# Performance work log

Hardware: AMD Instinct MI355X
Metric: run time of the kernel (lower is better)

The kernel has to match this reference:

```python
import jax, jax.numpy as jnp
import numpy as np

D_MODEL = 512
NUM_HEADS = 8
WINDOW = 64
HEAD_DIM = D_MODEL // NUM_HEADS


def setup_inputs() -> dict:
    key = jax.random.key(0)
    k1, k2, k3 = jax.random.split(key, 3)
    B, F, L, D = 4, 16, 2048, D_MODEL
    x = jax.random.normal(k1, (B, F, L, D), dtype=jnp.float32)
    w_qkv = jax.random.normal(k2, (D, 3 * D), dtype=jnp.float32) * (1.0 / np.sqrt(D))
    b_qkv = jnp.zeros((3 * D,), dtype=jnp.float32)
    w_proj = jax.random.normal(k3, (D, D), dtype=jnp.float32) * (1.0 / np.sqrt(D))
    b_proj = jnp.zeros((D,), dtype=jnp.float32)
    return {"x": x, "w_qkv": w_qkv, "b_qkv": b_qkv, "w_proj": w_proj, "b_proj": b_proj}


def reference(x, w_qkv, b_qkv, w_proj, b_proj):
    B, F, L, D = x.shape
    W = WINDOW
    H, hd = NUM_HEADS, HEAD_DIM
    nw = L // W  # L chosen divisible by window_size; pad path is identity here
    # partition into windows: (B, F, nw, W, D)
    xw = x.reshape(B, F, nw, W, D)
    # fused QKV projection
    qkv = jnp.einsum('bfnwd,de->bfnwe', xw, w_qkv) + b_qkv  # (B,F,nw,W,3D)
    qkv = qkv.reshape(B, F, nw, W, 3, H, hd)
    q = qkv[..., 0, :, :]  # (B,F,nw,W,H,hd)
    k = qkv[..., 1, :, :]
    v = qkv[..., 2, :, :]
    scale = 1.0 / np.sqrt(hd).astype(np.float32)
    # per-window attention: scores (B,F,nw,H,W,W)
    scores = jnp.einsum('bfnqhd,bfnkhd->bfnhqk', q, k) * scale
    attn = jax.nn.softmax(scores, axis=-1)
    out = jnp.einsum('bfnhqk,bfnkhd->bfnqhd', attn, v)  # (B,F,nw,W,H,hd)
    out = out.reshape(B, F, nw, W, D)
    out = jnp.einsum('bfnwd,de->bfnwe', out, w_proj) + b_proj
    return out.reshape(B, F, L, D)
```

## Files before the change

kernel.cpp:

```cpp
#include <hip/hip_runtime.h>

typedef __attribute__((ext_vector_type(8))) short short8;
typedef __attribute__((ext_vector_type(4))) float f32x4;
typedef unsigned short u16;
typedef unsigned int u32;

__device__ __forceinline__ u16 f2bf(float f){
  union { float f; u32 u; } v; v.f = f;
  u32 u = v.u;
  u32 r = (u + 0x7FFFu + ((u >> 16) & 1u)) >> 16;
  return (u16)r;
}

__device__ __forceinline__ u32 cvtpk(float a, float b){
  u32 r;
  asm("v_cvt_pk_bf16_f32 %0, %1, %2" : "=v"(r) : "v"(a), "v"(b));
  return r;
}

__device__ __forceinline__ int swz(int row, int cb){ return cb ^ ((row & 7) << 4); }

__device__ __forceinline__ void gload16(const void* g, void* l){
  __builtin_amdgcn_global_load_lds(
      (const __attribute__((address_space(1))) unsigned int*)g,
      (__attribute__((address_space(3))) unsigned int*)l, 16, 0, 0);
}

__global__ void convert_weights_swz(const float* __restrict__ wqkv,
                                    const float* __restrict__ wproj,
                                    u16* __restrict__ wq_swz,
                                    u16* __restrict__ wpt){
  int c = blockIdx.x * 256 + threadIdx.x;
  union { u16 u[8]; uint4 v; } t;
  if (c < 98304){
    int tile = c >> 10, row = (c >> 3) & 127, c7 = c & 7;
    int bn = tile >> 3, kt = tile & 7;
    int j  = c7 ^ (row & 7);
    int e  = bn * 128 + row;
    int k0 = kt * 64 + j * 8;
    #pragma unroll
    for (int i = 0; i < 8; ++i) t.u[i] = f2bf(wqkv[(long)(k0 + i) * 1536 + e]);
    *reinterpret_cast<uint4*>(wq_swz + (long)c * 8) = t.v;
  } else {
    int t2 = c - 98304;
    int cc = t2 >> 6;
    int kc = (t2 & 63) << 3;
    #pragma unroll
    for (int i = 0; i < 8; ++i) t.u[i] = f2bf(wproj[(long)(kc + i) * 512 + cc]);
    *reinterpret_cast<uint4*>(wpt + (long)cc * 512 + kc) = t.v;
  }
}

__global__ void convert_x(const float* __restrict__ x, u16* __restrict__ xbf){
  int c = blockIdx.x * 256 + threadIdx.x;
  int tile = c >> 10, row = (c >> 3) & 127, c7 = c & 7;
  int bm = tile >> 3, kt = tile & 7;
  int j  = c7 ^ (row & 7);
  const float* src = x + (long)(bm * 128 + row) * 512 + kt * 64 + j * 8;
  float4 v0 = *reinterpret_cast<const float4*>(src);
  float4 v1 = *reinterpret_cast<const float4*>(src + 4);
  union { u16 u[8]; uint4 v; } t;
  t.u[0] = f2bf(v0.x); t.u[1] = f2bf(v0.y); t.u[2] = f2bf(v0.z); t.u[3] = f2bf(v0.w);
  t.u[4] = f2bf(v1.x); t.u[5] = f2bf(v1.y); t.u[6] = f2bf(v1.z); t.u[7] = f2bf(v1.w);
  *reinterpret_cast<uint4*>(xbf + (long)c * 8) = t.v;
}

__global__ __launch_bounds__(256) void qkv_gemm(
    const u16*  __restrict__ xbf,
    const u16*  __restrict__ wswz,
    const float* __restrict__ bqkv,
    u16* __restrict__ qkv)
{
  __shared__ char smem[34816];
  char* ldsA = smem;
  char* ldsB = smem + 16384;
  u16*  ldsC = (u16*)smem;

  int hb   = blockIdx.x;
  int work = (hb & 7) * 1536 + (hb >> 3);
  int bn   = work % 12;
  int bm   = work / 12;

  const int tid = threadIdx.x;
  const int l = tid & 63, w = tid >> 6;
  const int g = l >> 4,  ln = l & 15;
  const int wm = w >> 1, wn = w & 1;

  f32x4 acc[4][4];
  #pragma unroll
  for (int m = 0; m < 4; ++m)
    #pragma unroll
    for (int n = 0; n < 4; ++n) acc[m][n] = (f32x4){0.f,0.f,0.f,0.f};

  const char* abase = (const char*)(xbf  + (long)(bm * 8) * 8192);
  const char* bbase = (const char*)(wswz + (long)(bn * 8) * 8192);

  for (int kt = 0; kt < 8; ++kt){
    __syncthreads();
    #pragma unroll
    for (int i = 0; i < 4; ++i){
      gload16(abase + (long)kt*16384 + (i*256 + tid)*16, ldsA + (i*256 + w*64)*16);
      gload16(bbase + (long)kt*16384 + (i*256 + tid)*16, ldsB + (i*256 + w*64)*16);
    }
    __syncthreads();
    #pragma unroll
    for (int ks = 0; ks < 2; ++ks){
      short8 a[4], b[4];
      #pragma unroll
      for (int m = 0; m < 4; ++m){
        int row = wm*64 + m*16 + ln;
        a[m] = *reinterpret_cast<const short8*>(ldsA + row*128 + (((ks*4 + g) ^ (row & 7)) << 4));
      }
      #pragma unroll
      for (int n = 0; n < 4; ++n){
        int row = wn*64 + n*16 + ln;
        b[n] = *reinterpret_cast<const short8*>(ldsB + row*128 + (((ks*4 + g) ^ (row & 7)) << 4));
      }
      #pragma unroll
      for (int m = 0; m < 4; ++m)
        #pragma unroll
        for (int n = 0; n < 4; ++n)
          acc[m][n] = __builtin_amdgcn_mfma_f32_16x16x32_bf16(a[m], b[n], acc[m][n], 0, 0, 0);
    }
  }

  __syncthreads();
  #pragma unroll
  for (int n = 0; n < 4; ++n){
    int col  = wn*64 + n*16 + ln;
    float bias = bqkv[bn*128 + col];
    #pragma unroll
    for (int m = 0; m < 4; ++m){
      int r0 = wm*64 + m*16 + g*4;
      #pragma unroll
      for (int r = 0; r < 4; ++r)
        ldsC[(r0 + r) * 136 + col] = f2bf(acc[m][n][r] + bias);
    }
  }
  __syncthreads();
  {
    int row = tid >> 1, half = tid & 1;
    const char* src = (const char*)(ldsC + row * 136 + half * 64);
    char* dst = (char*)qkv + ((long)(bm*128 + row) * 1536 + bn*128 + half*64) * 2;
    #pragma unroll
    for (int j = 0; j < 8; ++j)
      *reinterpret_cast<uint4*>(dst + j*16) = *reinterpret_cast<const uint4*>(src + j*16);
  }
}

__global__ __launch_bounds__(512, 4) void winattn_proj(
    const u16* __restrict__ qkv,
    const u16* __restrict__ wpt,
    const float* __restrict__ bproj,
    float* __restrict__ out)
{
  __shared__ u16 lds[8][4096];
  const int tid = threadIdx.x;
  const int l = tid & 63, w = tid >> 6;
  const int g = l >> 4,  ln = l & 15;
  const int gh = g >> 1, gl = g & 1;
  const long tokb = (long)blockIdx.x * 64;
  u16* vt = lds[w];
  const int h = w;

  {
    const int dg = l & 3, tg = l >> 2;
    uint4 vr[4][2];
    #pragma unroll
    for (int r = 0; r < 4; ++r){
      const char* vrow = (const char*)(qkv + (tokb + tg*4 + r) * 1536 + 1024 + h*64 + dg*16);
      vr[r][0] = *reinterpret_cast<const uint4*>(vrow);
      vr[r][1] = *reinterpret_cast<const uint4*>(vrow + 16);
    }
    #pragma unroll
    for (int dd = 0; dd < 16; ++dd){
      int d = dg*16 + dd;
      int sub = dd & 7, hi = dd >> 3;
      uint2 pk;
      pk.x = (u32)((const u16*)&vr[0][hi])[sub] | ((u32)((const u16*)&vr[1][hi])[sub] << 16);
      pk.y = (u32)((const u16*)&vr[2][hi])[sub] | ((u32)((const u16*)&vr[3][hi])[sub] << 16);
      *reinterpret_cast<uint2*>((char*)vt + d*128 + swz(d, tg*8)) = pk;
    }
  }

  f32x4 oacc[4][4];
  #pragma unroll
  for (int m = 0; m < 4; ++m)
    #pragma unroll
    for (int n = 0; n < 4; ++n) oacc[m][n] = (f32x4){0.f,0.f,0.f,0.f};

  const int lnA = ln + 32*gl;

  #pragma unroll
  for (int half = 0; half < 2; ++half){
    short8 qa[2][2];
    #pragma unroll
    for (int j = 0; j < 2; ++j){
      const char* qrow = (const char*)(qkv + (tokb + (half*2+j)*16 + ln) * 1536 + h*64 + g*8);
      qa[j][0] = *reinterpret_cast<const short8*>(qrow);
      qa[j][1] = *reinterpret_cast<const short8*>(qrow + 64);
    }
    f32x4 st[4][2];
    #pragma unroll
    for (int mk = 0; mk < 4; ++mk){
      st[mk][0] = (f32x4){0.f,0.f,0.f,0.f};
      st[mk][1] = (f32x4){0.f,0.f,0.f,0.f};
    }
    #pragma unroll
    for (int mk = 0; mk < 4; ++mk){
      const char* krow = (const char*)(qkv + (tokb + mk*16 + ln) * 1536 + 512 + h*64 + g*8);
      short8 kb0 = *reinterpret_cast<const short8*>(krow);
      short8 kb1 = *reinterpret_cast<const short8*>(krow + 64);
      #pragma unroll
      for (int j = 0; j < 2; ++j){
        st[mk][j] = __builtin_amdgcn_mfma_f32_16x16x32_bf16(kb0, qa[j][0], st[mk][j], 0, 0, 0);
        st[mk][j] = __builtin_amdgcn_mfma_f32_16x16x32_bf16(kb1, qa[j][1], st[mk][j], 0, 0, 0);
      }
    }
    u32 warr[4][2][2];
    #pragma unroll
    for (int j = 0; j < 2; ++j){
      float mx = -3.4e38f;
      #pragma unroll
      for (int mk = 0; mk < 4; ++mk)
        #pragma unroll
        for (int r = 0; r < 4; ++r) mx = fmaxf(mx, st[mk][j][r]);
      mx = fmaxf(mx, __shfl_xor(mx, 16, 64));
      mx = fmaxf(mx, __shfl_xor(mx, 32, 64));
      float s = 0.f;
      #pragma unroll
      for (int mk = 0; mk < 4; ++mk)
        #pragma unroll
        for (int r = 0; r < 4; ++r){
          float p = __expf((st[mk][j][r] - mx) * 0.125f);
          st[mk][j][r] = p; s += p;
        }
      s += __shfl_xor(s, 16, 64);
      s += __shfl_xor(s, 32, 64);
      float inv = 1.f / s;
      #pragma unroll
      for (int mk = 0; mk < 4; ++mk){
        warr[mk][j][0] = cvtpk(st[mk][j][0]*inv, st[mk][j][1]*inv);
        warr[mk][j][1] = cvtpk(st[mk][j][2]*inv, st[mk][j][3]*inv);
      }
    }
    __builtin_amdgcn_s_setprio(1);
    #pragma unroll
    for (int ks = 0; ks < 2; ++ks){
      short8 vb[4];
      #pragma unroll
      for (int n = 0; n < 4; ++n){
        int row = n*16 + ln;
        vb[n] = *reinterpret_cast<const short8*>((char*)vt + row*128 + swz(row, (ks*32 + g*8)*2));
      }
      #pragma unroll
      for (int mo = 0; mo < 2; ++mo){
        int m = half*2 + mo;
        u32 c0a = warr[2*ks  ][mo][0], c0b = warr[2*ks  ][mo][1];
        u32 c1a = warr[2*ks+1][mo][0], c1b = warr[2*ks+1][mo][1];
        u32 s0a = (u32)__shfl((int)c0a, lnA, 64);
        u32 s1a = (u32)__shfl((int)c1a, lnA, 64);
        u32 s0b = (u32)__shfl((int)c0b, lnA, 64);
        u32 s1b = (u32)__shfl((int)c1b, lnA, 64);
        u32 t0a = (u32)__shfl((int)c0a, lnA+16, 64);
        u32 t1a = (u32)__shfl((int)c1a, lnA+16, 64);
        u32 t0b = (u32)__shfl((int)c0b, lnA+16, 64);
        u32 t1b = (u32)__shfl((int)c1b, lnA+16, 64);
        union { u32 u[4]; short8 v; } pf;
        pf.u[0] = gh ? s1a : s0a;
        pf.u[1] = gh ? s1b : s0b;
        pf.u[2] = gh ? t1a : t0a;
        pf.u[3] = gh ? t1b : t0b;
        #pragma unroll
        for (int n = 0; n < 4; ++n)
          oacc[m][n] = __builtin_amdgcn_mfma_f32_16x16x32_bf16(pf.v, vb[n], oacc[m][n], 0, 0, 0);
      }
    }
    __builtin_amdgcn_s_setprio(0);
  }

  #pragma unroll
  for (int m = 0; m < 4; ++m)
    #pragma unroll
    for (int n = 0; n < 4; ++n){
      int d = n*16 + ln;
      #pragma unroll
      for (int r = 0; r < 4; ++r){
        int t = m*16 + g*4 + r;
        *reinterpret_cast<u16*>((char*)vt + t*128 + swz(t, d*2)) = f2bf(oacc[m][n][r]);
      }
    }

  __syncthreads();

  f32x4 acc[4][4];
  #pragma unroll
  for (int m = 0; m < 4; ++m)
    #pragma unroll
    for (int n = 0; n < 4; ++n) acc[m][n] = (f32x4){0.f,0.f,0.f,0.f};

  for (int hh = 0; hh < 8; ++hh){
    const char* obuf = (const char*)lds[hh];
    #pragma unroll
    for (int ks = 0; ks < 2; ++ks){
      short8 a[4], b[4];
      #pragma unroll
      for (int m = 0; m < 4; ++m){
        int row = m*16 + ln;
        a[m] = *reinterpret_cast<const short8*>(obuf + row*128 + swz(row, (ks*32 + g*8)*2));
      }
      #pragma unroll
      for (int n = 0; n < 4; ++n){
        int e = w*64 + n*16 + ln;
        b[n] = *reinterpret_cast<const short8*>(wpt + (long)e*512 + hh*64 + ks*32 + g*8);
      }
      __builtin_amdgcn_s_setprio(1);
      #pragma unroll
      for (int m = 0; m < 4; ++m)
        #pragma unroll
        for (int n = 0; n < 4; ++n)
          acc[m][n] = __builtin_amdgcn_mfma_f32_16x16x32_bf16(a[m], b[n], acc[m][n], 0, 0, 0);
      __builtin_amdgcn_s_setprio(0);
    }
  }

  #pragma unroll
  for (int n = 0; n < 4; ++n){
    int col = w*64 + n*16 + ln;
    float bias = bproj[col];
    #pragma unroll
    for (int m = 0; m < 4; ++m){
      #pragma unroll
      for (int r = 0; r < 4; ++r){
        int t = m*16 + g*4 + r;
        out[(tokb + t) * 512 + col] = acc[m][n][r] + bias;
      }
    }
  }
}

__global__ void convert_weights(const float* __restrict__ wqkv,
                                const float* __restrict__ wproj,
                                u16* __restrict__ wqkvt,
                                u16* __restrict__ wprojt){
  int tid = blockIdx.x * 256 + threadIdx.x;
  union { u16 u[8]; uint4 v; } tmp;
  if (tid < 1536 * 64){
    int e  = tid >> 6;
    int kc = (tid & 63) << 3;
    #pragma unroll
    for (int i = 0; i < 8; ++i) tmp.u[i] = f2bf(wqkv[(long)(kc + i) * 1536 + e]);
    *reinterpret_cast<uint4*>(wqkvt + (long)e * 512 + kc) = tmp.v;
  } else {
    int t2 = tid - 1536 * 64;
    int c  = t2 >> 6;
    int kc = (t2 & 63) << 3;
    #pragma unroll
    for (int i = 0; i < 8; ++i) tmp.u[i] = f2bf(wproj[(long)(kc + i) * 512 + c]);
    *reinterpret_cast<uint4*>(wprojt + (long)c * 512 + kc) = tmp.v;
  }
}

__global__ __launch_bounds__(512, 2) void fused_winattn(
    const float* __restrict__ x,
    const u16*  __restrict__ wqkvt,
    const float* __restrict__ bqkv,
    const u16*  __restrict__ wprojt,
    const float* __restrict__ bproj,
    float* __restrict__ out)
{
  __shared__ u16 lds_x[64 * 512];
  __shared__ u16 lds_q[64 * 64];
  __shared__ u16 lds_k[64 * 64];
  __shared__ u16 lds_vt[64 * 64];
  __shared__ u16 lds_p[64 * 64];

  const int tid = threadIdx.x;
  const int l   = tid & 63;
  const int w   = tid >> 6;
  const int g   = l >> 4;
  const int ln  = l & 15;
  const long tokbase = (long)blockIdx.x * 64;

  {
    const float4* xv = reinterpret_cast<const float4*>(x + tokbase * 512);
    #pragma unroll
    for (int j = 0; j < 16; ++j){
      int i   = j * 512 + tid;
      int row = i >> 7;
      int c4  = i & 127;
      float4 v = xv[i];
      uint2 pk;
      pk.x = (u32)f2bf(v.x) | ((u32)f2bf(v.y) << 16);
      pk.y = (u32)f2bf(v.z) | ((u32)f2bf(v.w) << 16);
      int byte = row * 1024 + swz(row, c4 * 8);
      *reinterpret_cast<uint2*>(reinterpret_cast<char*>(lds_x) + byte) = pk;
    }
  }

  f32x4 oacc[4][4];
  #pragma unroll
  for (int m = 0; m < 4; ++m)
    #pragma unroll
    for (int n = 0; n < 4; ++n) oacc[m][n] = (f32x4){0.f, 0.f, 0.f, 0.f};

  const int mw   = w & 3;
  const int half = w >> 2;

  __syncthreads();

  for (int h = 0; h < 8; ++h){
    f32x4 qacc[6];
    #pragma unroll
    for (int j = 0; j < 6; ++j) qacc[j] = (f32x4){0.f, 0.f, 0.f, 0.f};
    int ebase[6];
    #pragma unroll
    for (int j = 0; j < 6; ++j){
      int nt = half * 6 + j;
      int sec = nt >> 2;
      ebase[j] = sec * 512 + h * 64 + (nt & 3) * 16;
    }
    const int arow = mw * 16 + ln;
    #pragma unroll
    for (int ks = 0; ks < 16; ++ks){
      short8 a = *reinterpret_cast<const short8*>(
          reinterpret_cast<const char*>(lds_x) + arow * 1024 + swz(arow, (ks * 32 + g * 8) * 2));
      #pragma unroll
      for (int j = 0; j < 6; ++j){
        short8 b = *reinterpret_cast<const short8*>(
            wqkvt + (long)(ebase[j] + ln) * 512 + ks * 32 + g * 8);
        qacc[j] = __builtin_amdgcn_mfma_f32_16x16x32_bf16(a, b, qacc[j], 0, 0, 0);
      }
    }
    #pragma unroll
    for (int j = 0; j < 6; ++j){
      int nt  = half * 6 + j;
      int sec = nt >> 2;
      float bias = bqkv[ebase[j] + ln];
      if (sec < 2){
        u16* dst = (sec == 0) ? lds_q : lds_k;
        int c = (nt & 3) * 16 + ln;
        #pragma unroll
        for (int r = 0; r < 4; ++r){
          int t = mw * 16 + g * 4 + r;
          int byte = t * 128 + swz(t, c * 2);
          *reinterpret_cast<u16*>(reinterpret_cast<char*>(dst) + byte) = f2bf(qacc[j][r] + bias);
        }
      } else {
        int d  = (nt & 3) * 16 + ln;
        int t0 = mw * 16 + g * 4;
        uint2 pk;
        pk.x = (u32)f2bf(qacc[j][0] + bias) | ((u32)f2bf(qacc[j][1] + bias) << 16);
        pk.y = (u32)f2bf(qacc[j][2] + bias) | ((u32)f2bf(qacc[j][3] + bias) << 16);
        int byte = d * 128 + swz(d, t0 * 2);
        *reinterpret_cast<uint2*>(reinterpret_cast<char*>(lds_vt) + byte) = pk;
      }
    }
    __syncthreads();

    if (w < 4){
      f32x4 sacc[4];
      #pragma unroll
      for (int jt = 0; jt < 4; ++jt) sacc[jt] = (f32x4){0.f, 0.f, 0.f, 0.f};
      #pragma unroll
      for (int ks = 0; ks < 2; ++ks){
        int qrow = w * 16 + ln;
        short8 a = *reinterpret_cast<const short8*>(
            reinterpret_cast<const char*>(lds_q) + qrow * 128 + swz(qrow, (ks * 32 + g * 8) * 2));
        #pragma unroll
        for (int jt = 0; jt < 4; ++jt){
          int krow = jt * 16 + ln;
          short8 b = *reinterpret_cast<const short8*>(
              reinterpret_cast<const char*>(lds_k) + krow * 128 + swz(krow, (ks * 32 + g * 8) * 2));
          sacc[jt] = __builtin_amdgcn_mfma_f32_16x16x32_bf16(a, b, sacc[jt], 0, 0, 0);
        }
      }
      #pragma unroll
      for (int r = 0; r < 4; ++r){
        float mx = fmaxf(fmaxf(sacc[0][r], sacc[1][r]), fmaxf(sacc[2][r], sacc[3][r]));
        mx = fmaxf(mx, __shfl_xor(mx, 1, 64));
        mx = fmaxf(mx, __shfl_xor(mx, 2, 64));
        mx = fmaxf(mx, __shfl_xor(mx, 4, 64));
        mx = fmaxf(mx, __shfl_xor(mx, 8, 64));
        float p[4], s = 0.f;
        #pragma unroll
        for (int jt = 0; jt < 4; ++jt){
          p[jt] = __expf((sacc[jt][r] - mx) * 0.125f);
          s += p[jt];
        }
        s += __shfl_xor(s, 1, 64);
        s += __shfl_xor(s, 2, 64);
        s += __shfl_xor(s, 4, 64);
        s += __shfl_xor(s, 8, 64);
        float inv = 1.f / s;
        int i = w * 16 + g * 4 + r;
        #pragma unroll
        for (int jt = 0; jt < 4; ++jt){
          int c = jt * 16 + ln;
          int byte = i * 128 + swz(i, c * 2);
          *reinterpret_cast<u16*>(reinterpret_cast<char*>(lds_p) + byte) = f2bf(p[jt] * inv);
        }
      }
    }
    __syncthreads();

    {
      int mc  = w & 3;
      int nc0 = (w >> 2) * 2;
      f32x4 oc[2];
      oc[0] = (f32x4){0.f, 0.f, 0.f, 0.f};
      oc[1] = (f32x4){0.f, 0.f, 0.f, 0.f};
      #pragma unroll
      for (int ks = 0; ks < 2; ++ks){
        int prow = mc * 16 + ln;
        short8 a = *reinterpret_cast<const short8*>(
            reinterpret_cast<const char*>(lds_p) + prow * 128 + swz(prow, (ks * 32 + g * 8) * 2));
        #pragma unroll
        for (int jj = 0; jj < 2; ++jj){
          int vrow = (nc0 + jj) * 16 + ln;
          short8 b = *reinterpret_cast<const short8*>(
              reinterpret_cast<const char*>(lds_vt) + vrow * 128 + swz(vrow, (ks * 32 + g * 8) * 2));
          oc[jj] = __builtin_amdgcn_mfma_f32_16x16x32_bf16(a, b, oc[jj], 0, 0, 0);
        }
      }
      #pragma unroll
      for (int jj = 0; jj < 2; ++jj){
        int d = (nc0 + jj) * 16 + ln;
        #pragma unroll
        for (int r = 0; r < 4; ++r){
          int t = mc * 16 + g * 4 + r;
          int byte = t * 128 + swz(t, d * 2);
          *reinterpret_cast<u16*>(reinterpret_cast<char*>(lds_q) + byte) = f2bf(oc[jj][r]);
        }
      }
    }
    __syncthreads();

    #pragma unroll
    for (int ks = 0; ks < 2; ++ks){
      short8 a[4];
      #pragma unroll
      for (int m = 0; m < 4; ++m){
        int row = m * 16 + ln;
        a[m] = *reinterpret_cast<const short8*>(
            reinterpret_cast<const char*>(lds_q) + row * 128 + swz(row, (ks * 32 + g * 8) * 2));
      }
      #pragma unroll
      for (int nt = 0; nt < 4; ++nt){
        int e = w * 64 + nt * 16 + ln;
        short8 b = *reinterpret_cast<const short8*>(
            wprojt + (long)e * 512 + h * 64 + ks * 32 + g * 8);
        #pragma unroll
        for (int m = 0; m < 4; ++m)
          oacc[m][nt] = __builtin_amdgcn_mfma_f32_16x16x32_bf16(a[m], b, oacc[m][nt], 0, 0, 0);
      }
    }
    __syncthreads();
  }

  #pragma unroll
  for (int nt = 0; nt < 4; ++nt){
    int col = w * 64 + nt * 16 + ln;
    float bias = bproj[col];
    #pragma unroll
    for (int m = 0; m < 4; ++m){
      #pragma unroll
      for (int r = 0; r < 4; ++r){
        int t = m * 16 + g * 4 + r;
        out[(tokbase + t) * 512 + col] = oacc[m][nt][r] + bias;
      }
    }
  }
}

extern "C" void kernel_launch(void* const* d_in, const int* in_sizes, int n_in,
                              void* d_out, int out_size, void* d_ws, size_t ws_size,
                              hipStream_t stream) {
  const float* x     = (const float*)d_in[0];
  const float* wqkv  = (const float*)d_in[1];
  const float* bqkv  = (const float*)d_in[2];
  const float* wproj = (const float*)d_in[3];
  const float* bproj = (const float*)d_in[4];
  float* out = (float*)d_out;

  const size_t NEED = 538968064ULL;
  if (ws_size >= NEED){
    u16* wq_swz = (u16*)d_ws;
    u16* wpt    = (u16*)((char*)d_ws + 1572864);
    u16* xbf    = (u16*)((char*)d_ws + 2097152);
    u16* qkv    = (u16*)((char*)d_ws + 136314880);
    convert_weights_swz<<<512, 256, 0, stream>>>(wqkv, wproj, wq_swz, wpt);
    convert_x<<<32768, 256, 0, stream>>>(x, xbf);
    qkv_gemm<<<12288, 256, 0, stream>>>(xbf, wq_swz, bqkv, qkv);
    winattn_proj<<<2048, 512, 0, stream>>>(qkv, wpt, bproj, out);
  } else {
    u16* wqkvt  = (u16*)d_ws;
    u16* wprojt = wqkvt + 1536 * 512;
    convert_weights<<<512, 256, 0, stream>>>(wqkv, wproj, wqkvt, wprojt);
    fused_winattn<<<2048, 512, 0, stream>>>(x, wqkvt, bqkv, wprojt, bproj, out);
  }
}
```

Baseline: 662.6 us.

## Enlarge QKV GEMM tile to 256x256 with double-buffered LDS prefetch

Replaces the 128x128 QKV GEMM with a 512-thread 256x256 tile kernel that double-buffers A and B tiles in 128KB of LDS. Loads for the next K step are issued in slices between MFMA groups, and MFMA sections run at raised wave priority. Each tile is reused more, which cuts global and L2 traffic per FLOP and overlaps loads with compute. In exchange, the large LDS footprint and 128 accumulator registers limit occupancy to about one block per CU, and the epilogue is now split into two phases.

```diff
diff --git a/kernel.cpp b/kernel.cpp
--- a/kernel.cpp
+++ b/kernel.cpp
@@ -65,86 +65,122 @@
   *reinterpret_cast<uint4*>(xbf + (long)c * 8) = t.v;
 }
 
-__global__ __launch_bounds__(256) void qkv_gemm(
+__global__ __launch_bounds__(512, 2) void qkv_gemm256(
     const u16*  __restrict__ xbf,
     const u16*  __restrict__ wswz,
     const float* __restrict__ bqkv,
     u16* __restrict__ qkv)
 {
-  __shared__ char smem[34816];
-  char* ldsA = smem;
-  char* ldsB = smem + 16384;
-  u16*  ldsC = (u16*)smem;
-
-  int hb   = blockIdx.x;
-  int work = (hb & 7) * 1536 + (hb >> 3);
-  int bn   = work % 12;
-  int bm   = work / 12;
+  __shared__ char smem[131072];
 
   const int tid = threadIdx.x;
   const int l = tid & 63, w = tid >> 6;
   const int g = l >> 4,  ln = l & 15;
-  const int wm = w >> 1, wn = w & 1;
-
-  f32x4 acc[4][4];
-  #pragma unroll
-  for (int m = 0; m < 4; ++m)
+  const int wm = w >> 2, wn = w & 3;
+
+  int hb   = blockIdx.x;
+  int work = (hb & 7) * 384 + (hb >> 3);
+  int bn   = work % 6;
+  int bm   = work / 6;
+
+  f32x4 acc[8][4];
+  #pragma unroll
+  for (int m = 0; m < 8; ++m)
     #pragma unroll
     for (int n = 0; n < 4; ++n) acc[m][n] = (f32x4){0.f,0.f,0.f,0.f};
 
-  const char* abase = (const char*)(xbf  + (long)(bm * 8) * 8192);
-  const char* bbase = (const char*)(wswz + (long)(bn * 8) * 8192);
-
-  for (int kt = 0; kt < 8; ++kt){
+  auto stage_part = [&](int d, int kt, int p){
+    const char* src; char* dst;
+    if (p == 0){
+      src = (const char*)xbf  + ((long)(bm*2+0)*8 + kt)*16384;
+      dst = smem + d*32768;
+    } else if (p == 1){
+      src = (const char*)xbf  + ((long)(bm*2+1)*8 + kt)*16384;
+      dst = smem + d*32768 + 16384;
+    } else if (p == 2){
+      src = (const char*)wswz + ((long)(bn*2+0)*8 + kt)*16384;
+      dst = smem + 65536 + d*32768;
+    } else {
+      src = (const char*)wswz + ((long)(bn*2+1)*8 + kt)*16384;
+      dst = smem + 65536 + d*32768 + 16384;
+    }
+    gload16(src + (long)tid*16,         dst + w*1024);
+    gload16(src + (long)(512+tid)*16,   dst + 8192 + w*1024);
+  };
+
+  #pragma unroll
+  for (int p = 0; p < 4; ++p) stage_part(0, 0, p);
+  asm volatile("s_waitcnt vmcnt(0)");
+  __syncthreads();
+
+  const int brow0 = (wn & 1) * 64;
+  for (int t = 0; t < 8; ++t){
+    const int cur = t & 1;
+    const char* Abase = smem + cur*32768 + wm*16384;
+    const char* Bbase = smem + 65536 + cur*32768 + (wn >> 1)*16384;
+    #pragma unroll
+    for (int p = 0; p < 4; ++p){
+      if (t < 7) stage_part(cur^1, t+1, p);
+      const int mh = p >> 1, nh = p & 1;
+      short8 a[4][2], b[2][2];
+      #pragma unroll
+      for (int i = 0; i < 4; ++i){
+        int rowl = (mh*4 + i)*16 + ln;
+        #pragma unroll
+        for (int ks = 0; ks < 2; ++ks)
+          a[i][ks] = *reinterpret_cast<const short8*>(
+              Abase + rowl*128 + (((ks*4 + g) ^ (rowl & 7)) << 4));
+      }
+      #pragma unroll
+      for (int j = 0; j < 2; ++j){
+        int rowl = brow0 + (nh*2 + j)*16 + ln;
+        #pragma unroll
+        for (int ks = 0; ks < 2; ++ks)
+          b[j][ks] = *reinterpret_cast<const short8*>(
+              Bbase + rowl*128 + (((ks*4 + g) ^ (rowl & 7)) << 4));
+      }
+      __builtin_amdgcn_s_setprio(1);
+      #pragma unroll
+      for (int i = 0; i < 4; ++i)
+        #pragma unroll
+        for (int j = 0; j < 2; ++j)
+          #pragma unroll
+          for (int ks = 0; ks < 2; ++ks)
+            acc[mh*4+i][nh*2+j] = __builtin_amdgcn_mfma_f32_16x16x32_bf16(
+                a[i][ks], b[j][ks], acc[mh*4+i][nh*2+j], 0, 0, 0);
+      __builtin_amdgcn_s_setprio(0);
+    }
+    asm volatile("s_waitcnt vmcnt(0)" ::: "memory");
     __syncthreads();
-    #pragma unroll
-    for (int i = 0; i < 4; ++i){
-      gload16(abase + (long)kt*16384 + (i*256 + tid)*16, ldsA + (i*256 + w*64)*16);
-      gload16(bbase + (long)kt*16384 + (i*256 + tid)*16, ldsB + (i*256 + w*64)*16);
+  }
+
+  u16* ldsC = (u16*)smem;
+  #pragma unroll
+  for (int ph = 0; ph < 2; ++ph){
+    #pragma unroll
+    for (int mf = 0; mf < 4; ++mf){
+      int m = ph*4 + mf;
+      #pragma unroll
+      for (int n = 0; n < 4; ++n){
+        int col = wn*64 + n*16 + ln;
+        float bias = bqkv[bn*256 + col];
+        int lr0 = wm*64 + mf*16 + g*4;
+        #pragma unroll
+        for (int r = 0; r < 4; ++r)
+          ldsC[(lr0 + r)*264 + col] = f2bf(acc[m][n][r] + bias);
+      }
     }
     __syncthreads();
-    #pragma unroll
-    for (int ks = 0; ks < 2; ++ks){
-      short8 a[4], b[4];
-      #pragma unroll
-      for (int m = 0; m < 4; ++m){
-        int row = wm*64 + m*16 + ln;
-        a[m] = *reinterpret_cast<const short8*>(ldsA + row*128 + (((ks*4 + g) ^ (row & 7)) << 4));
-      }
-      #pragma unroll
-      for (int n = 0; n < 4; ++n){
-        int row = wn*64 + n*16 + ln;
-        b[n] = *reinterpret_cast<const short8*>(ldsB + row*128 + (((ks*4 + g) ^ (row & 7)) << 4));
-      }
-      #pragma unroll
-      for (int m = 0; m < 4; ++m)
-        #pragma unroll
-        for (int n = 0; n < 4; ++n)
-          acc[m][n] = __builtin_amdgcn_mfma_f32_16x16x32_bf16(a[m], b[n], acc[m][n], 0, 0, 0);
-    }
-  }
-
-  __syncthreads();
-  #pragma unroll
-  for (int n = 0; n < 4; ++n){
-    int col  = wn*64 + n*16 + ln;
-    float bias = bqkv[bn*128 + col];
-    #pragma unroll
-    for (int m = 0; m < 4; ++m){
-      int r0 = wm*64 + m*16 + g*4;
-      #pragma unroll
-      for (int r = 0; r < 4; ++r)
-        ldsC[(r0 + r) * 136 + col] = f2bf(acc[m][n][r] + bias);
-    }
-  }
-  __syncthreads();
-  {
-    int row = tid >> 1, half = tid & 1;
-    const char* src = (const char*)(ldsC + row * 136 + half * 64);
-    char* dst = (char*)qkv + ((long)(bm*128 + row) * 1536 + bn*128 + half*64) * 2;
-    #pragma unroll
-    for (int j = 0; j < 8; ++j)
-      *reinterpret_cast<uint4*>(dst + j*16) = *reinterpret_cast<const uint4*>(src + j*16);
+    {
+      int lr = tid >> 2, seg = tid & 3;
+      const char* src = (const char*)(ldsC + lr*264) + seg*128;
+      long gr = (long)bm*256 + (lr >> 6)*128 + ph*64 + (lr & 63);
+      char* dst = (char*)qkv + (gr*1536 + bn*256)*2 + seg*128;
+      #pragma unroll
+      for (int j = 0; j < 8; ++j)
+        *reinterpret_cast<uint4*>(dst + j*16) = *reinterpret_cast<const uint4*>(src + j*16);
+    }
+    __syncthreads();
   }
 }
 
@@ -591,7 +627,7 @@
     u16* qkv    = (u16*)((char*)d_ws + 136314880);
     convert_weights_swz<<<512, 256, 0, stream>>>(wqkv, wproj, wq_swz, wpt);
     convert_x<<<32768, 256, 0, stream>>>(x, xbf);
-    qkv_gemm<<<12288, 256, 0, stream>>>(xbf, wq_swz, bqkv, qkv);
+    qkv_gemm256<<<3072, 512, 0, stream>>>(xbf, wq_swz, bqkv, qkv);
     winattn_proj<<<2048, 512, 0, stream>>>(qkv, wpt, bproj, out);
   } else {
     u16* wqkvt  = (u16*)d_ws;
```

New measurement: 667.2 us. No clear change (+0.7%).

## Pre-lay weights in MFMA fragment order and double-buffer A tiles in QKV GEMM

Applied to the files above, without the earlier changes.

Weights are converted once into MFMA fragment order, so each lane loads its B operand directly from global memory as one contiguous 16-byte read instead of staging it through LDS. The QKV GEMM now double-buffers only the A tile in LDS with asynchronous global-to-LDS loads and manual waitcnt/barrier control, which overlaps the next tile's load with MFMA work. The projection in the attention kernel also reads weights in fragment order for coalesced access. The risk is more global/L2 traffic for B, which no longer gets reuse through LDS, and fragile hand-written vmcnt counts. Launch bounds now ask for three blocks per CU, which may limit registers.

```diff
diff --git a/kernel.cpp b/kernel.cpp
--- a/kernel.cpp
+++ b/kernel.cpp
@@ -26,28 +26,39 @@
       (__attribute__((address_space(3))) unsigned int*)l, 16, 0, 0);
 }
 
-__global__ void convert_weights_swz(const float* __restrict__ wqkv,
-                                    const float* __restrict__ wproj,
-                                    u16* __restrict__ wq_swz,
-                                    u16* __restrict__ wpt){
+__global__ void convert_weights_frag(const float* __restrict__ wqkv,
+                                     const float* __restrict__ wproj,
+                                     u16* __restrict__ wqf,
+                                     u16* __restrict__ wpf){
   int c = blockIdx.x * 256 + threadIdx.x;
   union { u16 u[8]; uint4 v; } t;
   if (c < 98304){
-    int tile = c >> 10, row = (c >> 3) & 127, c7 = c & 7;
-    int bn = tile >> 3, kt = tile & 7;
-    int j  = c7 ^ (row & 7);
-    int e  = bn * 128 + row;
-    int k0 = kt * 64 + j * 8;
+    int bn = c >> 13;
+    int r  = c & 8191;
+    int kt = r >> 10;
+    int q  = r & 1023;
+    int nsub = q >> 7;
+    int ks = (q >> 6) & 1;
+    int l  = q & 63;
+    int e  = bn*128 + nsub*16 + (l & 15);
+    int k0 = kt*64 + ks*32 + (l >> 4)*8;
     #pragma unroll
     for (int i = 0; i < 8; ++i) t.u[i] = f2bf(wqkv[(long)(k0 + i) * 1536 + e]);
-    *reinterpret_cast<uint4*>(wq_swz + (long)c * 8) = t.v;
+    *reinterpret_cast<uint4*>(wqf + (long)c * 8) = t.v;
   } else {
-    int t2 = c - 98304;
-    int cc = t2 >> 6;
-    int kc = (t2 & 63) << 3;
-    #pragma unroll
-    for (int i = 0; i < 8; ++i) t.u[i] = f2bf(wproj[(long)(kc + i) * 512 + cc]);
-    *reinterpret_cast<uint4*>(wpt + (long)cc * 512 + kc) = t.v;
+    int c2 = c - 98304;
+    int cb = c2 >> 12;
+    int r  = c2 & 4095;
+    int hh = r >> 9;
+    int q  = r & 511;
+    int n  = q >> 7;
+    int ks = (q >> 6) & 1;
+    int l  = q & 63;
+    int e  = cb*64 + n*16 + (l & 15);
+    int k0 = hh*64 + ks*32 + (l >> 4)*8;
+    #pragma unroll
+    for (int i = 0; i < 8; ++i) t.u[i] = f2bf(wproj[(long)(k0 + i) * 512 + e]);
+    *reinterpret_cast<uint4*>(wpf + (long)c2 * 8) = t.v;
   }
 }
 
@@ -65,66 +76,82 @@
   *reinterpret_cast<uint4*>(xbf + (long)c * 8) = t.v;
 }
 
-__global__ __launch_bounds__(256) void qkv_gemm(
+__global__ __launch_bounds__(256, 3) void qkv_gemm128(
     const u16*  __restrict__ xbf,
-    const u16*  __restrict__ wswz,
+    const u16*  __restrict__ wqf,
     const float* __restrict__ bqkv,
     u16* __restrict__ qkv)
 {
   __shared__ char smem[34816];
-  char* ldsA = smem;
-  char* ldsB = smem + 16384;
-  u16*  ldsC = (u16*)smem;
+
+  const int tid = threadIdx.x;
+  const int l = tid & 63, w = tid >> 6;
+  const int g = l >> 4,  ln = l & 15;
+  const int wm = w >> 1, wn = w & 1;
 
   int hb   = blockIdx.x;
   int work = (hb & 7) * 1536 + (hb >> 3);
   int bn   = work % 12;
   int bm   = work / 12;
 
-  const int tid = threadIdx.x;
-  const int l = tid & 63, w = tid >> 6;
-  const int g = l >> 4,  ln = l & 15;
-  const int wm = w >> 1, wn = w & 1;
-
   f32x4 acc[4][4];
   #pragma unroll
   for (int m = 0; m < 4; ++m)
     #pragma unroll
     for (int n = 0; n < 4; ++n) acc[m][n] = (f32x4){0.f,0.f,0.f,0.f};
 
-  const char* abase = (const char*)(xbf  + (long)(bm * 8) * 8192);
-  const char* bbase = (const char*)(wswz + (long)(bn * 8) * 8192);
-
-  for (int kt = 0; kt < 8; ++kt){
-    __syncthreads();
-    #pragma unroll
-    for (int i = 0; i < 4; ++i){
-      gload16(abase + (long)kt*16384 + (i*256 + tid)*16, ldsA + (i*256 + w*64)*16);
-      gload16(bbase + (long)kt*16384 + (i*256 + tid)*16, ldsB + (i*256 + w*64)*16);
-    }
-    __syncthreads();
-    #pragma unroll
-    for (int ks = 0; ks < 2; ++ks){
-      short8 a[4], b[4];
-      #pragma unroll
-      for (int m = 0; m < 4; ++m){
-        int row = wm*64 + m*16 + ln;
-        a[m] = *reinterpret_cast<const short8*>(ldsA + row*128 + (((ks*4 + g) ^ (row & 7)) << 4));
-      }
-      #pragma unroll
-      for (int n = 0; n < 4; ++n){
-        int row = wn*64 + n*16 + ln;
-        b[n] = *reinterpret_cast<const short8*>(ldsB + row*128 + (((ks*4 + g) ^ (row & 7)) << 4));
-      }
-      #pragma unroll
-      for (int m = 0; m < 4; ++m)
-        #pragma unroll
-        for (int n = 0; n < 4; ++n)
-          acc[m][n] = __builtin_amdgcn_mfma_f32_16x16x32_bf16(a[m], b[n], acc[m][n], 0, 0, 0);
-    }
-  }
-
-  __syncthreads();
+  const char* abase = (const char*)(xbf + (long)(bm * 8) * 8192);
+  const u16*  bbase = wqf + (long)bn * 65536;
+
+  auto stageA = [&](int kt, int slot){
+    const char* src = abase + (long)kt * 16384;
+    char* dst = smem + slot * 16384;
+    #pragma unroll
+    for (int i = 0; i < 4; ++i)
+      gload16(src + (i*256 + tid)*16, dst + i*4096 + w*1024);
+  };
+
+  stageA(0, 0); stageA(1, 1);
+  asm volatile("s_waitcnt vmcnt(4)" ::: "memory");
+  __builtin_amdgcn_s_barrier();
+
+  for (int t = 0; t < 8; ++t){
+    short8 b[4][2];
+    #pragma unroll
+    for (int n = 0; n < 4; ++n)
+      #pragma unroll
+      for (int ks = 0; ks < 2; ++ks)
+        b[n][ks] = *reinterpret_cast<const short8*>(
+            bbase + ((((long)t*8 + wn*4 + n)*2 + ks)*64 + l)*8);
+    const char* Ab = smem + (t & 1) * 16384;
+    short8 a[4][2];
+    #pragma unroll
+    for (int m = 0; m < 4; ++m){
+      int r = wm*64 + m*16 + ln;
+      #pragma unroll
+      for (int ks = 0; ks < 2; ++ks)
+        a[m][ks] = *reinterpret_cast<const short8*>(
+            Ab + r*128 + (((ks*4 + g) ^ (r & 7)) << 4));
+    }
+    asm volatile("s_waitcnt lgkmcnt(0)" ::: "memory");
+    __builtin_amdgcn_s_barrier();
+    if (t < 6) stageA(t + 2, t & 1);
+    __builtin_amdgcn_s_setprio(1);
+    #pragma unroll
+    for (int m = 0; m < 4; ++m)
+      #pragma unroll
+      for (int n = 0; n < 4; ++n)
+        #pragma unroll
+        for (int ks = 0; ks < 2; ++ks)
+          acc[m][n] = __builtin_amdgcn_mfma_f32_16x16x32_bf16(
+              a[m][ks], b[n][ks], acc[m][n], 0, 0, 0);
+    __builtin_amdgcn_s_setprio(0);
+    if (t < 6)       asm volatile("s_waitcnt vmcnt(4)" ::: "memory");
+    else if (t == 6) asm volatile("s_waitcnt vmcnt(0)" ::: "memory");
+    if (t < 7) __builtin_amdgcn_s_barrier();
+  }
+
+  u16* ldsC = (u16*)smem;
   #pragma unroll
   for (int n = 0; n < 4; ++n){
     int col  = wn*64 + n*16 + ln;
@@ -150,7 +177,7 @@
 
 __global__ __launch_bounds__(512, 4) void winattn_proj(
     const u16* __restrict__ qkv,
-    const u16* __restrict__ wpt,
+    const u16* __restrict__ wpf,
     const float* __restrict__ bproj,
     float* __restrict__ out)
 {
@@ -310,10 +337,9 @@
         a[m] = *reinterpret_cast<const short8*>(obuf + row*128 + swz(row, (ks*32 + g*8)*2));
       }
       #pragma unroll
-      for (int n = 0; n < 4; ++n){
-        int e = w*64 + n*16 + ln;
-        b[n] = *reinterpret_cast<const short8*>(wpt + (long)e*512 + hh*64 + ks*32 + g*8);
-      }
+      for (int n = 0; n < 4; ++n)
+        b[n] = *reinterpret_cast<const short8*>(
+            wpf + ((((long)w*8 + hh)*4 + n)*2 + ks)*512 + (long)l*8);
       __builtin_amdgcn_s_setprio(1);
       #pragma unroll
       for (int m = 0; m < 4; ++m)
@@ -585,14 +611,14 @@
 
   const size_t NEED = 538968064ULL;
   if (ws_size >= NEED){
-    u16* wq_swz = (u16*)d_ws;
-    u16* wpt    = (u16*)((char*)d_ws + 1572864);
-    u16* xbf    = (u16*)((char*)d_ws + 2097152);
-    u16* qkv    = (u16*)((char*)d_ws + 136314880);
-    convert_weights_swz<<<512, 256, 0, stream>>>(wqkv, wproj, wq_swz, wpt);
+    u16* wqf = (u16*)d_ws;
+    u16* wpf = (u16*)((char*)d_ws + 1572864);
+    u16* xbf = (u16*)((char*)d_ws + 2097152);
+    u16* qkv = (u16*)((char*)d_ws + 136314880);
+    convert_weights_frag<<<512, 256, 0, stream>>>(wqkv, wproj, wqf, wpf);
     convert_x<<<32768, 256, 0, stream>>>(x, xbf);
-    qkv_gemm<<<12288, 256, 0, stream>>>(xbf, wq_swz, bqkv, qkv);
-    winattn_proj<<<2048, 512, 0, stream>>>(qkv, wpt, bproj, out);
+    qkv_gemm128<<<12288, 256, 0, stream>>>(xbf, wqf, bqkv, qkv);
+    winattn_proj<<<2048, 512, 0, stream>>>(qkv, wpf, bproj, out);
   } else {
     u16* wqkvt  = (u16*)d_ws;
     u16* wprojt = wqkvt + 1536 * 512;
```

Measured after the change: 582.6 us, median of 3. 1.14x faster.
